# Kernel optimization log

Measured on AMD Instinct MI355X. Metric: run time of the kernel, lower is better.

Reference implementation:

```python
import jax, jax.numpy as jnp
import numpy as np

EPS = 1e-8

def _penalty(v, lo, hi):
    # if v<lo: (lo-v)/lo ; elif v>hi (hi finite): (v-hi)/hi ; else 0
    below = (lo - v) / lo
    if np.isinf(hi):
        return jnp.where(v < lo, below, 0.0)
    above = (v - hi) / hi
    return jnp.where(v < lo, below, jnp.where(v > hi, above, 0.0))

def _symbolic_features(x):
    # x: [B, input_dim]; column mapping from the original per-row loop
    am, bod, do, ph, nit = x[:, 0], x[:, 1], x[:, 2], x[:, 4], x[:, 7]
    # penalties in param_order = [ph, ammonia, bod, dissolved_oxygen, nitrate]
    p_ph  = _penalty(ph, 6.5, 8.5)
    p_am  = _penalty(am, 0.001, 0.5)
    p_bod = _penalty(bod, 0.001, 5.0)
    p_do  = _penalty(do, 6.0, np.inf)
    p_nit = _penalty(nit, 0.001, 10.0)
    # pollutant scores (missing params like 'nitrogen'/'orthophosphate' are skipped -> count adjusts)
    s_bact = (1.2 * am / (0.5 + EPS) + 1.5 * bod / (5.0 + EPS) - 0.8 * do / (10.0 + EPS)) / 3.0
    s_chem = (1.5 * ph / (8.5 + EPS) + 1.0 * nit / (10.0 + EPS)) / 2.0
    s_org  = (2.0 * bod / (5.0 + EPS) - 1.5 * do / (10.0 + EPS) + 0.8 * am / (0.5 + EPS)) / 3.0
    s_agr  = (2.0 * nit / (10.0 + EPS)) / 1.0
    resil = 1.0 / (1.0 + (p_ph + p_am + p_bod + p_do + p_nit) + EPS)
    return jnp.stack([p_ph, p_am, p_bod, p_do, p_nit, s_bact, s_chem, s_org, s_agr, resil], axis=1)

def setup_inputs() -> dict:
    key = jax.random.key(0)
    ks = jax.random.split(key, 16)
    B, D_IN, SYM, H = 1048576, 10, 10, 64
    def lin(k, fin, fout):
        k1, k2 = jax.random.split(k)
        s = 1.0 / np.sqrt(fin)
        return (jax.random.uniform(k1, (fin, fout), jnp.float32, -s, s),
                jax.random.uniform(k2, (fout,), jnp.float32, -s, s))
    W_sym, b_sym = lin(ks[0], SYM, H // 2)
    W_in, b_in = lin(ks[1], D_IN + H // 2, H)
    W1, b1 = lin(ks[2], H, H)
    W2, b2 = lin(ks[3], H, H)
    W3, b3 = lin(ks[4], H, H)
    W_r1, b_r1 = lin(ks[5], H, H // 2)
    W_r2, b_r2 = lin(ks[6], H // 2, 1)
    W_c1, b_c1 = lin(ks[7], H, H // 2)
    W_c2, b_c2 = lin(ks[8], H // 2, 4)
    x = jax.random.uniform(ks[9], (B, D_IN), jnp.float32)
    return {"x": x, "W_sym": W_sym, "b_sym": b_sym, "W_in": W_in, "b_in": b_in,
            "W1": W1, "b1": b1, "W2": W2, "b2": b2, "W3": W3, "b3": b3,
            "W_r1": W_r1, "b_r1": b_r1, "W_r2": W_r2, "b_r2": b_r2,
            "W_c1": W_c1, "b_c1": b_c1, "W_c2": W_c2, "b_c2": b_c2}

def reference(x, W_sym, b_sym, W_in, b_in, W1, b1, W2, b2, W3, b3,
              W_r1, b_r1, W_r2, b_r2, W_c1, b_c1, W_c2, b_c2):
    elu = jax.nn.elu
    sym = _symbolic_features(x)                      # [B, 10]
    sym_enc = elu(sym @ W_sym + b_sym)               # [B, 32]  (Dropout: eval mode = identity)
    h = elu(jnp.concatenate([x, sym_enc], axis=1) @ W_in + b_in)  # [B, 64]
    for W, b in ((W1, b1), (W2, b2), (W3, b3)):
        h = h + elu(h @ W + b)                       # residual MLP stack
    predictions = elu(h @ W_r1 + b_r1) @ W_r2 + b_r2            # [B, 1]
    pollutant_logits = elu(h @ W_c1 + b_c1) @ W_c2 + b_c2       # [B, 4]
    return predictions, pollutant_logits
```

## Files before the change

### kernel.cpp

```cpp
#include <hip/hip_runtime.h>
#include <hip/hip_bf16.h>
#include <math.h>

#define NROWS 1048576
#define EPSF 1e-8f

typedef unsigned short ushortT;
typedef __attribute__((ext_vector_type(8))) short short8;
typedef __attribute__((ext_vector_type(4))) short short4v;
typedef __attribute__((ext_vector_type(4))) float floatx4;
typedef __attribute__((ext_vector_type(2))) int int2v;

#define WS_HI   256
#define WS_LO   41216
#define WS_MF   82176
#define MF_B5   0
#define MF_WSYM 320
#define MF_BSYM 640
#define MF_WR2  672
#define MF_BR2  704
#define MF_WC2  708
#define MF_BC2  836
#define MF_WC2T 840

#define LDS_FENCE() asm volatile("s_waitcnt lgkmcnt(0)" ::: "memory")

struct WPtrs { const void* p[19]; };

__global__ void sniff_kernel(const ushortT* __restrict__ x, int* __restrict__ flag) {
    if (threadIdx.x == 0 && blockIdx.x == 0) {
        unsigned s = 0;
        for (int i = 0; i < 64; ++i) s |= (unsigned)(x[i] & 0x8000u);
        *flag = s ? 1 : 0;
    }
}

__device__ __forceinline__ float ldw(const void* p, int i, bool f32) {
    return f32 ? ((const float*)p)[i]
               : __uint_as_float(((unsigned)((const ushortT*)p)[i]) << 16);
}

__global__ void prep_kernel(WPtrs wp, const int* __restrict__ flag, void* __restrict__ ws) {
    const bool f32 = (*flag != 0);
    ushortT* hi = (ushortT*)((char*)ws + WS_HI);
    ushortT* lo = (ushortT*)((char*)ws + WS_LO);
    float* mf = (float*)((char*)ws + WS_MF);
    const int B = blockIdx.x;
    if (B < 5) {
        const int L = B;
        for (int idx = threadIdx.x; idx < 4096; idx += 256) {
            const int j8 = idx & 7, ln = (idx >> 3) & 63, s2 = (idx >> 9) & 1, t = idx >> 10;
            const int s = 2 * s2 + (j8 >> 2), j = j8 & 3;
            const int k = 16 * s + 4 * (ln >> 4) + j;
            const int m = 16 * t + (ln & 15);
            float w = 0.0f;
            if (L == 0)      { if (k < 42) w = ldw(wp.p[3], k * 64 + m, f32); }
            else if (L <= 3) { if (k < 64) w = ldw(wp.p[3 + 2 * L], k * 64 + m, f32); }
            else             { if (k < 64) w = (m < 32) ? ldw(wp.p[11], k * 32 + m, f32)
                                                        : ldw(wp.p[15], k * 32 + (m - 32), f32); }
            const unsigned u = __float_as_uint(w);
            const float rem = w - __uint_as_float(u & 0xffff0000u);
            hi[L * 4096 + idx] = (ushortT)(u >> 16);
            lo[L * 4096 + idx] = (ushortT)(__float_as_uint(rem) >> 16);
        }
    } else {
        const int src[12] = {4, 6, 8, 10, 12, 16, 1, 2, 13, 14, 17, 18};
        const int cnt[12] = {64, 64, 64, 64, 32, 32, 320, 32, 32, 1, 128, 4};
        const int dst[12] = {0, 64, 128, 192, 256, 288, MF_WSYM, MF_BSYM, MF_WR2, MF_BR2, MF_WC2, MF_BC2};
        for (int a = 0; a < 12; ++a)
            for (int i = threadIdx.x; i < cnt[a]; i += 256)
                mf[dst[a] + i] = ldw(wp.p[src[a]], i, f32);
        for (int i = threadIdx.x; i < 128; i += 256) {
            const int qq = i >> 5, j = i & 31;
            mf[MF_WC2T + i] = ldw(wp.p[17], j * 4 + qq, f32);
        }
    }
}

__device__ __forceinline__ float eluf(float v) {
    return fmaxf(v, 0.0f) + (__expf(fminf(v, 0.0f)) - 1.0f);
}

__device__ __forceinline__ unsigned pack_hi16(unsigned ua, unsigned ub) {
    return __builtin_amdgcn_perm(ub, ua, 0x07060302u);
}

__device__ __forceinline__ void split4(float a0, float a1, float a2, float a3,
                                       short4v& h4, short4v& l4) {
    const unsigned u0 = __float_as_uint(a0), u1 = __float_as_uint(a1);
    const unsigned u2 = __float_as_uint(a2), u3 = __float_as_uint(a3);
    int2v h, l;
    h[0] = (int)pack_hi16(u0, u1);
    h[1] = (int)pack_hi16(u2, u3);
    const float l0 = a0 - __uint_as_float(u0 & 0xffff0000u);
    const float l1 = a1 - __uint_as_float(u1 & 0xffff0000u);
    const float l2 = a2 - __uint_as_float(u2 & 0xffff0000u);
    const float l3 = a3 - __uint_as_float(u3 & 0xffff0000u);
    l[0] = (int)pack_hi16(__float_as_uint(l0), __float_as_uint(l1));
    l[1] = (int)pack_hi16(__float_as_uint(l2), __float_as_uint(l3));
    h4 = __builtin_bit_cast(short4v, h);
    l4 = __builtin_bit_cast(short4v, l);
}

__device__ __forceinline__ floatx4 mfma16(short4v a, short4v b, floatx4 c) {
#if __has_builtin(__builtin_amdgcn_mfma_f32_16x16x16bf16_1k)
    return __builtin_amdgcn_mfma_f32_16x16x16bf16_1k(a, b, c, 0, 0, 0);
#else
    floatx4 d;
    asm("v_mfma_f32_16x16x16_bf16 %0, %1, %2, %3" : "=v"(d) : "v"(a), "v"(b), "v"(c));
    return d;
#endif
}

template<bool F32>
__device__ __forceinline__ void run_body(
    const void* __restrict__ xin, const char* __restrict__ wsb,
    void* __restrict__ out, float (* __restrict__ hb)[68],
    const int lane, const int rowg)
{
    const ushortT* __restrict__ wfhi = (const ushortT*)(wsb + WS_HI);
    const ushortT* __restrict__ wflo = (const ushortT*)(wsb + WS_LO);
    const float* __restrict__ mf = (const float*)(wsb + WS_MF);
    const int n = lane & 15, q = lane >> 4;

    float x[10];
    if (F32) {
        const float* xp = (const float*)xin + (size_t)rowg * 10;
        #pragma unroll
        for (int i = 0; i < 10; ++i) x[i] = xp[i];
    } else {
        const unsigned* xd = (const unsigned*)((const ushortT*)xin + (size_t)rowg * 10);
        #pragma unroll
        for (int i = 0; i < 5; ++i) {
            const unsigned d = xd[i];
            x[2 * i]     = __uint_as_float(d << 16);
            x[2 * i + 1] = __uint_as_float(d & 0xffff0000u);
        }
    }
    if (q == 0) {
        #pragma unroll
        for (int i = 0; i < 10; ++i) hb[n][i] = x[i];
    }
    #pragma unroll
    for (int i = 0; i < 6; ++i) {
        const int c = 42 + q * 6 + i;
        if (c < 64) hb[n][c] = 0.0f;
    }

    const float am = x[0], bod = x[1], dox = x[2], ph = x[4], nit = x[7];
    const float p_ph  = ph  < 6.5f   ? (6.5f - ph) * 0.15384616f
                      : (ph > 8.5f   ? (ph - 8.5f) * 0.11764706f : 0.0f);
    const float p_am  = am  < 0.001f ? (0.001f - am) * 1000.0f
                      : (am > 0.5f   ? (am - 0.5f) * 2.0f : 0.0f);
    const float p_bod = bod < 0.001f ? (0.001f - bod) * 1000.0f
                      : (bod > 5.0f  ? (bod - 5.0f) * 0.2f : 0.0f);
    const float p_do  = dox < 6.0f   ? (6.0f - dox) * 0.16666667f : 0.0f;
    const float p_nit = nit < 0.001f ? (0.001f - nit) * 1000.0f
                      : (nit > 10.0f ? (nit - 10.0f) * 0.1f : 0.0f);
    const float s_bact = (am * 2.3999999f + bod * 0.29999998f - dox * 0.08f) * 0.33333334f;
    const float s_chem = (ph * 0.17647059f + nit * 0.1f) * 0.5f;
    const float s_org  = (bod * 0.39999998f - dox * 0.14999999f + am * 1.5999999f) * 0.33333334f;
    const float s_agr  = nit * 0.2f;
    const float resil  = 1.0f / (1.0f + (p_ph + p_am + p_bod + p_do + p_nit) + EPSF);
    const float sym[10] = {p_ph, p_am, p_bod, p_do, p_nit, s_bact, s_chem, s_org, s_agr, resil};

    float se[8];
    {
        const floatx4 b0 = *(const floatx4*)(mf + MF_BSYM + q * 8);
        const floatx4 b1 = *(const floatx4*)(mf + MF_BSYM + q * 8 + 4);
        #pragma unroll
        for (int jj = 0; jj < 4; ++jj) { se[jj] = b0[jj]; se[4 + jj] = b1[jj]; }
        #pragma unroll
        for (int k = 0; k < 10; ++k) {
            const floatx4 w0 = *(const floatx4*)(mf + MF_WSYM + k * 32 + q * 8);
            const floatx4 w1 = *(const floatx4*)(mf + MF_WSYM + k * 32 + q * 8 + 4);
            #pragma unroll
            for (int jj = 0; jj < 4; ++jj) {
                se[jj]     = fmaf(sym[k], w0[jj], se[jj]);
                se[4 + jj] = fmaf(sym[k], w1[jj], se[4 + jj]);
            }
        }
    }
    #pragma unroll
    for (int jj = 0; jj < 8; ++jj) hb[n][10 + q * 8 + jj] = eluf(se[jj]);
    LDS_FENCE();

    short4v Bhi[4], Blo[4];
    #pragma unroll
    for (int s = 0; s < 4; ++s) {
        const floatx4 v = *(const floatx4*)&hb[n][16 * s + 4 * q];
        split4(v[0], v[1], v[2], v[3], Bhi[s], Blo[s]);
    }

    float hprev[4][4];
    float z[4][4];
    #pragma unroll
    for (int L = 0; L < 5; ++L) {
        floatx4 acc[4];
        #pragma unroll
        for (int t = 0; t < 4; ++t)
            acc[t] = *(const floatx4*)(mf + MF_B5 + L * 64 + 16 * t + 4 * q);
        #pragma unroll
        for (int s2 = 0; s2 < 2; ++s2) {
            #pragma unroll
            for (int t = 0; t < 4; ++t) {
                const int off = L * 4096 + (t * 2 + s2) * 512 + lane * 8;
                const short8 Ap = *(const short8*)(wfhi + off);
                const short4v ae = {Ap[0], Ap[1], Ap[2], Ap[3]};
                const short4v ao = {Ap[4], Ap[5], Ap[6], Ap[7]};
                acc[t] = mfma16(ae, Bhi[2 * s2],     acc[t]);
                acc[t] = mfma16(ae, Blo[2 * s2],     acc[t]);
                acc[t] = mfma16(ao, Bhi[2 * s2 + 1], acc[t]);
                acc[t] = mfma16(ao, Blo[2 * s2 + 1], acc[t]);
                if (F32) {
                    const short8 Alp = *(const short8*)(wflo + off);
                    const short4v le = {Alp[0], Alp[1], Alp[2], Alp[3]};
                    const short4v lo_ = {Alp[4], Alp[5], Alp[6], Alp[7]};
                    acc[t] = mfma16(le,  Bhi[2 * s2],     acc[t]);
                    acc[t] = mfma16(lo_, Bhi[2 * s2 + 1], acc[t]);
                }
            }
        }
        if (L < 4) {
            #pragma unroll
            for (int t = 0; t < 4; ++t) {
                #pragma unroll
                for (int r = 0; r < 4; ++r) {
                    const float e = eluf(acc[t][r]);
                    hprev[t][r] = (L >= 1) ? hprev[t][r] + e : e;
                }
                split4(hprev[t][0], hprev[t][1], hprev[t][2], hprev[t][3], Bhi[t], Blo[t]);
            }
        } else {
            #pragma unroll
            for (int t = 0; t < 4; ++t)
                #pragma unroll
                for (int r = 0; r < 4; ++r)
                    z[t][r] = eluf(acc[t][r]);
        }
    }

    float pred = (q == 0) ? mf[MF_BR2] : 0.0f;
    #pragma unroll
    for (int t = 0; t < 2; ++t) {
        const floatx4 w = *(const floatx4*)(mf + MF_WR2 + 16 * t + 4 * q);
        #pragma unroll
        for (int r = 0; r < 4; ++r) pred = fmaf(z[t][r], w[r], pred);
    }
    float lg[4];
    #pragma unroll
    for (int c = 0; c < 4; ++c) {
        lg[c] = (q == 0) ? mf[MF_BC2 + c] : 0.0f;
        #pragma unroll
        for (int t = 0; t < 2; ++t) {
            const floatx4 w = *(const floatx4*)(mf + MF_WC2T + c * 32 + 16 * t + 4 * q);
            #pragma unroll
            for (int r = 0; r < 4; ++r) lg[c] = fmaf(z[2 + t][r], w[r], lg[c]);
        }
    }
    pred += __shfl_xor(pred, 16, 64);
    pred += __shfl_xor(pred, 32, 64);
    #pragma unroll
    for (int c = 0; c < 4; ++c) {
        lg[c] += __shfl_xor(lg[c], 16, 64);
        lg[c] += __shfl_xor(lg[c], 32, 64);
    }
    const float lsel = q == 0 ? lg[0] : (q == 1 ? lg[1] : (q == 2 ? lg[2] : lg[3]));

    if (F32) {
        float* o = (float*)out;
        if (q == 0) o[rowg] = pred;
        o[NROWS + rowg * 4 + q] = lsel;
    } else {
        __hip_bfloat16* o = (__hip_bfloat16*)out;
        if (q == 0) o[rowg] = __float2bfloat16(pred);
        o[NROWS + rowg * 4 + q] = __float2bfloat16(lsel);
    }
}

__global__ __launch_bounds__(256, 4) void mlp_mfma_kernel(
    const void* __restrict__ xin, const int* __restrict__ flagp,
    const void* __restrict__ ws, void* __restrict__ out)
{
    __shared__ float hball[4][16][68];
    const int tid = threadIdx.x;
    const int wave = tid >> 6, lane = tid & 63;
    const int rowg = blockIdx.x * 64 + wave * 16 + (lane & 15);
    if (*flagp != 0)
        run_body<true>(xin, (const char*)ws, out, hball[wave], lane, rowg);
    else
        run_body<false>(xin, (const char*)ws, out, hball[wave], lane, rowg);
}

extern "C" void kernel_launch(void* const* d_in, const int* in_sizes, int n_in,
                              void* d_out, int out_size, void* d_ws, size_t ws_size,
                              hipStream_t stream) {
    (void)in_sizes; (void)n_in; (void)out_size; (void)ws_size;
    int* flag = (int*)d_ws;

    sniff_kernel<<<1, 64, 0, stream>>>((const ushortT*)d_in[0], flag);

    WPtrs wp;
    for (int i = 0; i < 19; ++i) wp.p[i] = d_in[i];
    prep_kernel<<<6, 256, 0, stream>>>(wp, flag, d_ws);

    mlp_mfma_kernel<<<NROWS / 64, 256, 0, stream>>>(d_in[0], flag, d_ws, d_out);
}
```

Baseline: 367.4 us.

## Process two 16-row tiles per wave to reuse loaded MFMA weight fragments

```diff
diff --git a/kernel.cpp b/kernel.cpp
--- a/kernel.cpp
+++ b/kernel.cpp
@@ -85,6 +85,10 @@
     return __builtin_amdgcn_perm(ub, ua, 0x07060302u);
 }
 
+__device__ __forceinline__ float b2f(short h) {
+    return __uint_as_float(((unsigned)(ushortT)h) << 16);
+}
+
 __device__ __forceinline__ void split4(float a0, float a1, float a2, float a3,
                                        short4v& h4, short4v& l4) {
     const unsigned u0 = __float_as_uint(a0), u1 = __float_as_uint(a1);
@@ -116,180 +120,218 @@
 __device__ __forceinline__ void run_body(
     const void* __restrict__ xin, const char* __restrict__ wsb,
     void* __restrict__ out, float (* __restrict__ hb)[68],
-    const int lane, const int rowg)
+    const int lane, const int rowbase)
 {
     const ushortT* __restrict__ wfhi = (const ushortT*)(wsb + WS_HI);
     const ushortT* __restrict__ wflo = (const ushortT*)(wsb + WS_LO);
     const float* __restrict__ mf = (const float*)(wsb + WS_MF);
     const int n = lane & 15, q = lane >> 4;
 
-    float x[10];
-    if (F32) {
-        const float* xp = (const float*)xin + (size_t)rowg * 10;
-        #pragma unroll
-        for (int i = 0; i < 10; ++i) x[i] = xp[i];
-    } else {
-        const unsigned* xd = (const unsigned*)((const ushortT*)xin + (size_t)rowg * 10);
-        #pragma unroll
-        for (int i = 0; i < 5; ++i) {
-            const unsigned d = xd[i];
-            x[2 * i]     = __uint_as_float(d << 16);
-            x[2 * i + 1] = __uint_as_float(d & 0xffff0000u);
-        }
+    short4v Bhi[2][4], Blo[2][4];
+
+    #pragma unroll
+    for (int u = 0; u < 2; ++u) {
+        const int rowg = rowbase + 16 * u + n;
+        float x[10];
+        if (F32) {
+            const float* xp = (const float*)xin + (size_t)rowg * 10;
+            #pragma unroll
+            for (int i = 0; i < 10; ++i) x[i] = xp[i];
+        } else {
+            const unsigned* xd = (const unsigned*)((const ushortT*)xin + (size_t)rowg * 10);
+            #pragma unroll
+            for (int i = 0; i < 5; ++i) {
+                const unsigned d = xd[i];
+                x[2 * i]     = __uint_as_float(d << 16);
+                x[2 * i + 1] = __uint_as_float(d & 0xffff0000u);
+            }
+        }
+        if (q == 0) {
+            #pragma unroll
+            for (int i = 0; i < 10; ++i) hb[n][i] = x[i];
+        }
+        if (u == 0) {
+            #pragma unroll
+            for (int i = 0; i < 6; ++i) {
+                const int c = 42 + q * 6 + i;
+                if (c < 64) hb[n][c] = 0.0f;
+            }
+        }
+
+        const float am = x[0], bod = x[1], dox = x[2], ph = x[4], nit = x[7];
+        const float p_ph  = ph  < 6.5f   ? (6.5f - ph) * 0.15384616f
+                          : (ph > 8.5f   ? (ph - 8.5f) * 0.11764706f : 0.0f);
+        const float p_am  = am  < 0.001f ? (0.001f - am) * 1000.0f
+                          : (am > 0.5f   ? (am - 0.5f) * 2.0f : 0.0f);
+        const float p_bod = bod < 0.001f ? (0.001f - bod) * 1000.0f
+                          : (bod > 5.0f  ? (bod - 5.0f) * 0.2f : 0.0f);
+        const float p_do  = dox < 6.0f   ? (6.0f - dox) * 0.16666667f : 0.0f;
+        const float p_nit = nit < 0.001f ? (0.001f - nit) * 1000.0f
+                          : (nit > 10.0f ? (nit - 10.0f) * 0.1f : 0.0f);
+        const float s_bact = (am * 2.3999999f + bod * 0.29999998f - dox * 0.08f) * 0.33333334f;
+        const float s_chem = (ph * 0.17647059f + nit * 0.1f) * 0.5f;
+        const float s_org  = (bod * 0.39999998f - dox * 0.14999999f + am * 1.5999999f) * 0.33333334f;
+        const float s_agr  = nit * 0.2f;
+        const float resil  = 1.0f / (1.0f + (p_ph + p_am + p_bod + p_do + p_nit) + EPSF);
+        const float sym[10] = {p_ph, p_am, p_bod, p_do, p_nit, s_bact, s_chem, s_org, s_agr, resil};
+
+        float se[8];
+        {
+            const floatx4 b0 = *(const floatx4*)(mf + MF_BSYM + q * 8);
+            const floatx4 b1 = *(const floatx4*)(mf + MF_BSYM + q * 8 + 4);
+            #pragma unroll
+            for (int jj = 0; jj < 4; ++jj) { se[jj] = b0[jj]; se[4 + jj] = b1[jj]; }
+            #pragma unroll
+            for (int k = 0; k < 10; ++k) {
+                const floatx4 w0 = *(const floatx4*)(mf + MF_WSYM + k * 32 + q * 8);
+                const floatx4 w1 = *(const floatx4*)(mf + MF_WSYM + k * 32 + q * 8 + 4);
+                #pragma unroll
+                for (int jj = 0; jj < 4; ++jj) {
+                    se[jj]     = fmaf(sym[k], w0[jj], se[jj]);
+                    se[4 + jj] = fmaf(sym[k], w1[jj], se[4 + jj]);
+                }
+            }
+        }
+        #pragma unroll
+        for (int jj = 0; jj < 8; ++jj) hb[n][10 + q * 8 + jj] = eluf(se[jj]);
+        LDS_FENCE();
+
+        #pragma unroll
+        for (int s = 0; s < 4; ++s) {
+            const floatx4 v = *(const floatx4*)&hb[n][16 * s + 4 * q];
+            split4(v[0], v[1], v[2], v[3], Bhi[u][s], Blo[u][s]);
+        }
+        LDS_FENCE();
     }
-    if (q == 0) {
-        #pragma unroll
-        for (int i = 0; i < 10; ++i) hb[n][i] = x[i];
-    }
-    #pragma unroll
-    for (int i = 0; i < 6; ++i) {
-        const int c = 42 + q * 6 + i;
-        if (c < 64) hb[n][c] = 0.0f;
-    }
-
-    const float am = x[0], bod = x[1], dox = x[2], ph = x[4], nit = x[7];
-    const float p_ph  = ph  < 6.5f   ? (6.5f - ph) * 0.15384616f
-                      : (ph > 8.5f   ? (ph - 8.5f) * 0.11764706f : 0.0f);
-    const float p_am  = am  < 0.001f ? (0.001f - am) * 1000.0f
-                      : (am > 0.5f   ? (am - 0.5f) * 2.0f : 0.0f);
-    const float p_bod = bod < 0.001f ? (0.001f - bod) * 1000.0f
-                      : (bod > 5.0f  ? (bod - 5.0f) * 0.2f : 0.0f);
-    const float p_do  = dox < 6.0f   ? (6.0f - dox) * 0.16666667f : 0.0f;
-    const float p_nit = nit < 0.001f ? (0.001f - nit) * 1000.0f
-                      : (nit > 10.0f ? (nit - 10.0f) * 0.1f : 0.0f);
-    const float s_bact = (am * 2.3999999f + bod * 0.29999998f - dox * 0.08f) * 0.33333334f;
-    const float s_chem = (ph * 0.17647059f + nit * 0.1f) * 0.5f;
-    const float s_org  = (bod * 0.39999998f - dox * 0.14999999f + am * 1.5999999f) * 0.33333334f;
-    const float s_agr  = nit * 0.2f;
-    const float resil  = 1.0f / (1.0f + (p_ph + p_am + p_bod + p_do + p_nit) + EPSF);
-    const float sym[10] = {p_ph, p_am, p_bod, p_do, p_nit, s_bact, s_chem, s_org, s_agr, resil};
-
-    float se[8];
-    {
-        const floatx4 b0 = *(const floatx4*)(mf + MF_BSYM + q * 8);
-        const floatx4 b1 = *(const floatx4*)(mf + MF_BSYM + q * 8 + 4);
-        #pragma unroll
-        for (int jj = 0; jj < 4; ++jj) { se[jj] = b0[jj]; se[4 + jj] = b1[jj]; }
-        #pragma unroll
-        for (int k = 0; k < 10; ++k) {
-            const floatx4 w0 = *(const floatx4*)(mf + MF_WSYM + k * 32 + q * 8);
-            const floatx4 w1 = *(const floatx4*)(mf + MF_WSYM + k * 32 + q * 8 + 4);
-            #pragma unroll
-            for (int jj = 0; jj < 4; ++jj) {
-                se[jj]     = fmaf(sym[k], w0[jj], se[jj]);
-                se[4 + jj] = fmaf(sym[k], w1[jj], se[4 + jj]);
-            }
-        }
-    }
-    #pragma unroll
-    for (int jj = 0; jj < 8; ++jj) hb[n][10 + q * 8 + jj] = eluf(se[jj]);
-    LDS_FENCE();
-
-    short4v Bhi[4], Blo[4];
-    #pragma unroll
-    for (int s = 0; s < 4; ++s) {
-        const floatx4 v = *(const floatx4*)&hb[n][16 * s + 4 * q];
-        split4(v[0], v[1], v[2], v[3], Bhi[s], Blo[s]);
-    }
-
-    float hprev[4][4];
-    float z[4][4];
+
     #pragma unroll
     for (int L = 0; L < 5; ++L) {
-        floatx4 acc[4];
-        #pragma unroll
-        for (int t = 0; t < 4; ++t)
-            acc[t] = *(const floatx4*)(mf + MF_B5 + L * 64 + 16 * t + 4 * q);
-        #pragma unroll
-        for (int s2 = 0; s2 < 2; ++s2) {
-            #pragma unroll
-            for (int t = 0; t < 4; ++t) {
-                const int off = L * 4096 + (t * 2 + s2) * 512 + lane * 8;
-                const short8 Ap = *(const short8*)(wfhi + off);
-                const short4v ae = {Ap[0], Ap[1], Ap[2], Ap[3]};
-                const short4v ao = {Ap[4], Ap[5], Ap[6], Ap[7]};
-                acc[t] = mfma16(ae, Bhi[2 * s2],     acc[t]);
-                acc[t] = mfma16(ae, Blo[2 * s2],     acc[t]);
-                acc[t] = mfma16(ao, Bhi[2 * s2 + 1], acc[t]);
-                acc[t] = mfma16(ao, Blo[2 * s2 + 1], acc[t]);
+        short8 Ap[8];
+        const int base = L * 4096 + lane * 8;
+        #pragma unroll
+        for (int c = 0; c < 8; ++c)
+            Ap[c] = *(const short8*)(wfhi + base + c * 512);
+        short8 Alp[8];
+        if (F32) {
+            #pragma unroll
+            for (int c = 0; c < 8; ++c)
+                Alp[c] = *(const short8*)(wflo + base + c * 512);
+        }
+
+        floatx4 acc[2][4];
+        #pragma unroll
+        for (int t = 0; t < 4; ++t) {
+            const floatx4 b = *(const floatx4*)(mf + MF_B5 + L * 64 + 16 * t + 4 * q);
+            acc[0][t] = b; acc[1][t] = b;
+        }
+        #pragma unroll
+        for (int t = 0; t < 4; ++t) {
+            #pragma unroll
+            for (int s2 = 0; s2 < 2; ++s2) {
+                const short8 A = Ap[t * 2 + s2];
+                const short4v ae = {A[0], A[1], A[2], A[3]};
+                const short4v ao = {A[4], A[5], A[6], A[7]};
+                #pragma unroll
+                for (int u = 0; u < 2; ++u) {
+                    acc[u][t] = mfma16(ae, Bhi[u][2 * s2],     acc[u][t]);
+                    acc[u][t] = mfma16(ae, Blo[u][2 * s2],     acc[u][t]);
+                    acc[u][t] = mfma16(ao, Bhi[u][2 * s2 + 1], acc[u][t]);
+                    acc[u][t] = mfma16(ao, Blo[u][2 * s2 + 1], acc[u][t]);
+                }
                 if (F32) {
-                    const short8 Alp = *(const short8*)(wflo + off);
-                    const short4v le = {Alp[0], Alp[1], Alp[2], Alp[3]};
-                    const short4v lo_ = {Alp[4], Alp[5], Alp[6], Alp[7]};
-                    acc[t] = mfma16(le,  Bhi[2 * s2],     acc[t]);
-                    acc[t] = mfma16(lo_, Bhi[2 * s2 + 1], acc[t]);
-                }
-            }
-        }
+                    const short8 Al = Alp[t * 2 + s2];
+                    const short4v le  = {Al[0], Al[1], Al[2], Al[3]};
+                    const short4v lo_ = {Al[4], Al[5], Al[6], Al[7]};
+                    #pragma unroll
+                    for (int u = 0; u < 2; ++u) {
+                        acc[u][t] = mfma16(le,  Bhi[u][2 * s2],     acc[u][t]);
+                        acc[u][t] = mfma16(lo_, Bhi[u][2 * s2 + 1], acc[u][t]);
+                    }
+                }
+            }
+        }
+
         if (L < 4) {
             #pragma unroll
-            for (int t = 0; t < 4; ++t) {
+            for (int u = 0; u < 2; ++u) {
+                #pragma unroll
+                for (int t = 0; t < 4; ++t) {
+                    float h[4];
+                    #pragma unroll
+                    for (int r = 0; r < 4; ++r) {
+                        float e = eluf(acc[u][t][r]);
+                        if (L >= 1) e += b2f(Bhi[u][t][r]) + b2f(Blo[u][t][r]);
+                        h[r] = e;
+                    }
+                    split4(h[0], h[1], h[2], h[3], Bhi[u][t], Blo[u][t]);
+                }
+            }
+        } else {
+            const floatx4 wr0 = *(const floatx4*)(mf + MF_WR2 + 4 * q);
+            const floatx4 wr1 = *(const floatx4*)(mf + MF_WR2 + 16 + 4 * q);
+            floatx4 wc0[4], wc1[4];
+            #pragma unroll
+            for (int c = 0; c < 4; ++c) {
+                wc0[c] = *(const floatx4*)(mf + MF_WC2T + c * 32 + 4 * q);
+                wc1[c] = *(const floatx4*)(mf + MF_WC2T + c * 32 + 16 + 4 * q);
+            }
+            #pragma unroll
+            for (int u = 0; u < 2; ++u) {
+                float pred = (q == 0) ? mf[MF_BR2] : 0.0f;
+                float z2[4], z3[4];
                 #pragma unroll
                 for (int r = 0; r < 4; ++r) {
-                    const float e = eluf(acc[t][r]);
-                    hprev[t][r] = (L >= 1) ? hprev[t][r] + e : e;
-                }
-                split4(hprev[t][0], hprev[t][1], hprev[t][2], hprev[t][3], Bhi[t], Blo[t]);
-            }
-        } else {
-            #pragma unroll
-            for (int t = 0; t < 4; ++t)
-                #pragma unroll
-                for (int r = 0; r < 4; ++r)
-                    z[t][r] = eluf(acc[t][r]);
+                    pred = fmaf(eluf(acc[u][0][r]), wr0[r], pred);
+                    pred = fmaf(eluf(acc[u][1][r]), wr1[r], pred);
+                    z2[r] = eluf(acc[u][2][r]);
+                    z3[r] = eluf(acc[u][3][r]);
+                }
+                float lg[4];
+                #pragma unroll
+                for (int c = 0; c < 4; ++c) {
+                    float l = (q == 0) ? mf[MF_BC2 + c] : 0.0f;
+                    #pragma unroll
+                    for (int r = 0; r < 4; ++r) {
+                        l = fmaf(z2[r], wc0[c][r], l);
+                        l = fmaf(z3[r], wc1[c][r], l);
+                    }
+                    lg[c] = l;
+                }
+                pred += __shfl_xor(pred, 16, 64);
+                pred += __shfl_xor(pred, 32, 64);
+                #pragma unroll
+                for (int c = 0; c < 4; ++c) {
+                    lg[c] += __shfl_xor(lg[c], 16, 64);
+                    lg[c] += __shfl_xor(lg[c], 32, 64);
+                }
+                const float lsel = q == 0 ? lg[0] : (q == 1 ? lg[1] : (q == 2 ? lg[2] : lg[3]));
+                const int rowg = rowbase + 16 * u + n;
+                if (F32) {
+                    float* o = (float*)out;
+                    if (q == 0) o[rowg] = pred;
+                    o[NROWS + rowg * 4 + q] = lsel;
+                } else {
+                    __hip_bfloat16* o = (__hip_bfloat16*)out;
+                    if (q == 0) o[rowg] = __float2bfloat16(pred);
+                    o[NROWS + rowg * 4 + q] = __float2bfloat16(lsel);
+                }
+            }
         }
     }
-
-    float pred = (q == 0) ? mf[MF_BR2] : 0.0f;
-    #pragma unroll
-    for (int t = 0; t < 2; ++t) {
-        const floatx4 w = *(const floatx4*)(mf + MF_WR2 + 16 * t + 4 * q);
-        #pragma unroll
-        for (int r = 0; r < 4; ++r) pred = fmaf(z[t][r], w[r], pred);
-    }
-    float lg[4];
-    #pragma unroll
-    for (int c = 0; c < 4; ++c) {
-        lg[c] = (q == 0) ? mf[MF_BC2 + c] : 0.0f;
-        #pragma unroll
-        for (int t = 0; t < 2; ++t) {
-            const floatx4 w = *(const floatx4*)(mf + MF_WC2T + c * 32 + 16 * t + 4 * q);
-            #pragma unroll
-            for (int r = 0; r < 4; ++r) lg[c] = fmaf(z[2 + t][r], w[r], lg[c]);
-        }
-    }
-    pred += __shfl_xor(pred, 16, 64);
-    pred += __shfl_xor(pred, 32, 64);
-    #pragma unroll
-    for (int c = 0; c < 4; ++c) {
-        lg[c] += __shfl_xor(lg[c], 16, 64);
-        lg[c] += __shfl_xor(lg[c], 32, 64);
-    }
-    const float lsel = q == 0 ? lg[0] : (q == 1 ? lg[1] : (q == 2 ? lg[2] : lg[3]));
-
-    if (F32) {
-        float* o = (float*)out;
-        if (q == 0) o[rowg] = pred;
-        o[NROWS + rowg * 4 + q] = lsel;
-    } else {
-        __hip_bfloat16* o = (__hip_bfloat16*)out;
-        if (q == 0) o[rowg] = __float2bfloat16(pred);
-        o[NROWS + rowg * 4 + q] = __float2bfloat16(lsel);
-    }
-}
-
-__global__ __launch_bounds__(256, 4) void mlp_mfma_kernel(
+}
+
+__global__ __launch_bounds__(256, 2) void mlp_mfma_kernel(
     const void* __restrict__ xin, const int* __restrict__ flagp,
     const void* __restrict__ ws, void* __restrict__ out)
 {
     __shared__ float hball[4][16][68];
     const int tid = threadIdx.x;
     const int wave = tid >> 6, lane = tid & 63;
-    const int rowg = blockIdx.x * 64 + wave * 16 + (lane & 15);
+    const int rowbase = blockIdx.x * 128 + wave * 32;
     if (*flagp != 0)
-        run_body<true>(xin, (const char*)ws, out, hball[wave], lane, rowg);
+        run_body<true>(xin, (const char*)ws, out, hball[wave], lane, rowbase);
     else
-        run_body<false>(xin, (const char*)ws, out, hball[wave], lane, rowg);
+        run_body<false>(xin, (const char*)ws, out, hball[wave], lane, rowbase);
 }
 
 extern "C" void kernel_launch(void* const* d_in, const int* in_sizes, int n_in,
@@ -304,5 +346,5 @@
     for (int i = 0; i < 19; ++i) wp.p[i] = d_in[i];
     prep_kernel<<<6, 256, 0, stream>>>(wp, flag, d_ws);
 
-    mlp_mfma_kernel<<<NROWS / 64, 256, 0, stream>>>(d_in[0], flag, d_ws, d_out);
-}
+    mlp_mfma_kernel<<<NROWS / 128, 256, 0, stream>>>(d_in[0], flag, d_ws, d_out);
+}
```

New measurement: 371.6 us. Within noise of the previous version (+1.1%).
